# Kernel optimization log

Hardware: AMD Instinct MI355X
Metric: run time of the kernel (lower is better)

Reference implementation:

```python
import jax, jax.numpy as jnp
import numpy as np

THRESHOLD_FACTOR = 1.25
HIDDEN = 128
B, N = 4, 2048

def setup_inputs() -> dict:
    key = jax.random.key(0)
    ks = jax.random.split(key, 11)
    def lin(k, fin, fout):
        bound = 1.0 / np.sqrt(fin)
        kw, kb = jax.random.split(k)
        W = jax.random.uniform(kw, (fin, fout), jnp.float32, -bound, bound)
        b = jax.random.uniform(kb, (fout,), jnp.float32, -bound, bound)
        return W, b
    W1, b1 = lin(ks[0], 2, HIDDEN)
    W2, b2 = lin(ks[1], HIDDEN, HIDDEN)
    Wd, bd = lin(ks[2], HIDDEN, 1)
    Wr, br = lin(ks[3], HIDDEN, 1)
    Wm, bm = lin(ks[4], HIDDEN, 1)
    phase_coords = jax.random.normal(ks[5], (B, N, 2), jnp.float32)
    return dict(phase_coords=phase_coords, W1=W1, b1=b1, W2=W2, b2=b2,
                Wd=Wd, bd=bd, Wr=Wr, br=br, Wm=Wm, bm=bm)

def _attention(r):
    # diff[b,s,t,i] = r[b,s,i]*(-r[b,t,i]) + r[b,s,i] = r_s * (1 - r_t)
    diff = r[:, :, None, :] * (1.0 - r[:, None, :, :])        # [B,N,N,2]
    dist_sq = jnp.sum(diff * diff, axis=-1)                    # [B,N,N]
    phase_diff = jnp.arctan2(diff[..., 1], diff[..., 0])
    forward_bias = 0.5 * (1.0 + jnp.cos(phase_diff)) * jnp.exp(-dist_sq)
    mean_dist = jnp.mean(dist_sq, axis=(-1, -2), keepdims=True)
    std_dist = jnp.clip(jnp.std(dist_sq, axis=(-1, -2), keepdims=True, ddof=1), 1e-6, None)
    threshold = mean_dist + THRESHOLD_FACTOR * std_dist
    attn = jnp.where(dist_sq <= threshold, forward_bias, 0.0)
    row_sums = jnp.sum(attn, axis=-1, keepdims=True)
    return attn / (row_sums + 1e-8)

def reference(phase_coords, W1, b1, W2, b2, Wd, bd, Wr, br, Wm, bm):
    h = jax.nn.silu(phase_coords @ W1 + b1) @ W2 + b2           # [B,N,H]
    diffusion = h @ Wd + bd                                     # [B,N,1]
    reaction = h @ Wr + br
    migration = h @ Wm + bm
    attn = _attention(phase_coords)                             # [B,N,N]
    diffusion_field = jnp.einsum('bst,btk->bsk', attn, diffusion)
    return diffusion, reaction, migration, attn, diffusion_field
```

## Files before the change

kernel.cpp:

```cpp
#include <hip/hip_runtime.h>
#include <math.h>

#define NTOK 2048
#define HID  128
#define BB   4

typedef float f32x4 __attribute__((ext_vector_type(4)));

__device__ __forceinline__ float wave_red_f(float v) {
  #pragma unroll
  for (int o = 32; o; o >>= 1) v += __shfl_down(v, o, 64);
  return v;
}
__device__ __forceinline__ double wave_red_d(double v) {
  #pragma unroll
  for (int o = 32; o; o >>= 1) v += __shfl_down(v, o, 64);
  return v;
}

__global__ __launch_bounds__(256) void mlp_thr_kernel(
    const float* __restrict__ pc,
    const float* __restrict__ W1, const float* __restrict__ b1,
    const float* __restrict__ W2, const float* __restrict__ b2,
    const float* __restrict__ Wd, const float* __restrict__ bd,
    const float* __restrict__ Wr, const float* __restrict__ br,
    const float* __restrict__ Wm, const float* __restrict__ bm,
    float* __restrict__ outd, float* __restrict__ outr, float* __restrict__ outm,
    float* __restrict__ thr)
{
  const int tid = threadIdx.x;

  if (blockIdx.x >= 32) {
    const int wave = tid >> 6, lane = tid & 63;
    const int b = blockIdx.x - 32;
    const float2* r = (const float2*)(pc + (size_t)b * NTOK * 2);
    double m[10];
    #pragma unroll
    for (int j = 0; j < 10; ++j) m[j] = 0.0;
    for (int i = tid; i < NTOK; i += 256) {
      const float2 c = r[i];
      const double a = c.x, bq = c.y, u = 1.0 - (double)c.x, v = 1.0 - (double)c.y;
      const double a2 = a * a, b2v = bq * bq, u2 = u * u, v2 = v * v;
      m[0] += a2;       m[1] += b2v;
      m[2] += a2 * a2;  m[3] += b2v * b2v;  m[4] += a2 * b2v;
      m[5] += u2;       m[6] += v2;
      m[7] += u2 * u2;  m[8] += v2 * v2;    m[9] += u2 * v2;
    }
    #pragma unroll
    for (int j = 0; j < 10; ++j) m[j] = wave_red_d(m[j]);
    __shared__ double sm[4][10];
    if (lane == 0) {
      #pragma unroll
      for (int j = 0; j < 10; ++j) sm[wave][j] = m[j];
    }
    __syncthreads();
    if (tid == 0) {
      double t[10];
      #pragma unroll
      for (int j = 0; j < 10; ++j)
        t[j] = sm[0][j] + sm[1][j] + sm[2][j] + sm[3][j];
      const double Sq  = t[0] * t[5] + t[1] * t[6];
      const double Sqq = t[2] * t[7] + 2.0 * t[4] * t[9] + t[3] * t[8];
      const double M = (double)NTOK * (double)NTOK;
      const double mean = Sq / M;
      double var = (Sqq - Sq * Sq / M) / (M - 1.0);
      if (var < 0.0) var = 0.0;
      double sd = sqrt(var);
      if (sd < 1e-6) sd = 1e-6;
      thr[b] = (float)(mean + 1.25 * sd);
    }
    return;
  }

  __shared__ float fw[3][HID];
  __shared__ float fc[3];

  for (int idx = tid; idx < 3 * HID; idx += 256) {
    const int head = idx >> 7, k = idx & (HID - 1);
    const float* wh = (head == 0) ? Wd : (head == 1) ? Wr : Wm;
    const float4* w2row = (const float4*)(W2 + k * HID);
    const float4* wh4   = (const float4*)wh;
    float s = 0.f;
    #pragma unroll 4
    for (int j = 0; j < HID / 4; ++j) {
      const float4 a = w2row[j], w = wh4[j];
      s = fmaf(a.x, w.x, fmaf(a.y, w.y, fmaf(a.z, w.z, fmaf(a.w, w.w, s))));
    }
    fw[head][k] = s;
  }
  if (tid < 3) {
    const float* wh = (tid == 0) ? Wd : (tid == 1) ? Wr : Wm;
    const float bh  = (tid == 0) ? bd[0] : (tid == 1) ? br[0] : bm[0];
    const float4* b24 = (const float4*)b2;
    const float4* wh4 = (const float4*)wh;
    float s = 0.f;
    for (int j = 0; j < HID / 4; ++j) {
      const float4 a = b24[j], w = wh4[j];
      s = fmaf(a.x, w.x, fmaf(a.y, w.y, fmaf(a.z, w.z, fmaf(a.w, w.w, s))));
    }
    fc[tid] = s + bh;
  }
  __syncthreads();

  const int row = blockIdx.x * 256 + tid;
  const float2 c = ((const float2*)pc)[row];
  const float x0 = c.x, x1 = c.y;

  float dd = 0.f, rv = 0.f, mv = 0.f;
  #pragma unroll 4
  for (int k = 0; k < HID; ++k) {
    const float z = fmaf(x0, W1[k], fmaf(x1, W1[HID + k], b1[k]));
    const float h = z * __builtin_amdgcn_rcpf(1.f + __builtin_amdgcn_exp2f(-1.442695041f * z));
    dd = fmaf(h, fw[0][k], dd);
    rv = fmaf(h, fw[1][k], rv);
    mv = fmaf(h, fw[2][k], mv);
  }
  outd[row] = dd + fc[0];
  outr[row] = rv + fc[1];
  outm[row] = mv + fc[2];
}

__global__ __launch_bounds__(256) void attn_kernel(
    const float* __restrict__ pc, const float* __restrict__ diffu,
    const float* __restrict__ thr,
    float* __restrict__ attn, float* __restrict__ dfield)
{
  const int b = blockIdx.y;
  const int wave = threadIdx.x >> 6, lane = threadIdx.x & 63;
  const int s = blockIdx.x * 4 + wave;

  const float2* __restrict__ rr  = (const float2*)(pc + (size_t)b * NTOK * 2);
  const float4* __restrict__ rr4 = (const float4*)rr;
  const float4* __restrict__ sd4 = (const float4*)(diffu + b * NTOK);

  const float C = 1.2011224f;
  float2 u[32];
  float  sdr[32];
  #pragma unroll
  for (int j = 0; j < 8; ++j) {
    const float4 c0 = rr4[lane * 2 + j * 128];
    const float4 c1 = rr4[lane * 2 + 1 + j * 128];
    u[j * 4 + 0] = make_float2(C * (1.f - c0.x), C * (1.f - c0.y));
    u[j * 4 + 1] = make_float2(C * (1.f - c0.z), C * (1.f - c0.w));
    u[j * 4 + 2] = make_float2(C * (1.f - c1.x), C * (1.f - c1.y));
    u[j * 4 + 3] = make_float2(C * (1.f - c1.z), C * (1.f - c1.w));
    const float4 dv = sd4[lane + j * 64];
    sdr[j * 4 + 0] = dv.x; sdr[j * 4 + 1] = dv.y;
    sdr[j * 4 + 2] = dv.z; sdr[j * 4 + 3] = dv.w;
  }

  const float Ts = thr[b] * 1.442695041f;
  const float2 rc = rr[s];

  float v[32];
  float rsum = 0.f, dot = 0.f;
  #pragma unroll
  for (int k = 0; k < 32; ++k) {
    const float d0 = rc.x * u[k].x;
    const float d1 = rc.y * u[k].y;
    const float q = fmaf(d0, d0, d1 * d1);
    float val = 0.f;
    if (q <= Ts)
      val = (q > 0.f)
          ? fmaf(d0 * rsqrtf(q), 0.5f, 0.5f) * __builtin_amdgcn_exp2f(-q)
          : 1.f;
    v[k] = val;
    rsum += val;
    dot = fmaf(val, sdr[k], dot);
  }

  #pragma unroll
  for (int o = 1; o < 64; o <<= 1) {
    rsum += __shfl_xor(rsum, o, 64);
    dot  += __shfl_xor(dot, o, 64);
  }
  const float sc = 1.f / (rsum + 1e-8f);

  f32x4* arow4 = (f32x4*)(attn + ((size_t)b * NTOK + s) * NTOK);
  #pragma unroll
  for (int j = 0; j < 8; ++j) {
    f32x4 o;
    o.x = v[j * 4 + 0] * sc; o.y = v[j * 4 + 1] * sc;
    o.z = v[j * 4 + 2] * sc; o.w = v[j * 4 + 3] * sc;
    __builtin_nontemporal_store(o, arow4 + lane + j * 64);
  }
  if (lane == 0) dfield[b * NTOK + s] = dot * sc;
}

extern "C" void kernel_launch(void* const* d_in, const int* in_sizes, int n_in,
                              void* d_out, int out_size, void* d_ws, size_t ws_size,
                              hipStream_t stream) {
  const float* pc = (const float*)d_in[0];
  const float* W1 = (const float*)d_in[1];
  const float* b1 = (const float*)d_in[2];
  const float* W2 = (const float*)d_in[3];
  const float* b2 = (const float*)d_in[4];
  const float* Wd = (const float*)d_in[5];
  const float* bd = (const float*)d_in[6];
  const float* Wr = (const float*)d_in[7];
  const float* br = (const float*)d_in[8];
  const float* Wm = (const float*)d_in[9];
  const float* bm = (const float*)d_in[10];

  float* out    = (float*)d_out;
  float* outd   = out;
  float* outr   = out + BB * NTOK;
  float* outm   = out + 2 * BB * NTOK;
  float* attn   = out + 3 * BB * NTOK;
  float* dfield = attn + (size_t)BB * NTOK * NTOK;

  float* thr = (float*)d_ws;

  hipLaunchKernelGGL(mlp_thr_kernel, dim3(32 + BB), dim3(256), 0, stream,
                     pc, W1, b1, W2, b2, Wd, bd, Wr, br, Wm, bm,
                     outd, outr, outm, thr);
  hipLaunchKernelGGL(attn_kernel, dim3(NTOK / 4, BB), dim3(256), 0, stream,
                     pc, outd, thr, attn, dfield);
}
```

Measured before the change: 35.90 us.

## Split attention into row-stats pass and separate recompute-and-store pass

The fused attention kernel is split in two. A row-stats kernel computes the row sums and diffusion field and writes the per-row scale to a workspace buffer. A separate store kernel, with a flat grid-stride layout, recomputes every attention value and writes the normalized rows with plain stores instead of nontemporal ones. The aim is a cleaner, fully coalesced write stream for the 64 MB output, at the cost of computing each attention value twice and adding one kernel launch.

```diff
diff --git a/kernel.cpp b/kernel.cpp
--- a/kernel.cpp
+++ b/kernel.cpp
@@ -7,11 +7,6 @@
 
 typedef float f32x4 __attribute__((ext_vector_type(4)));
 
-__device__ __forceinline__ float wave_red_f(float v) {
-  #pragma unroll
-  for (int o = 32; o; o >>= 1) v += __shfl_down(v, o, 64);
-  return v;
-}
 __device__ __forceinline__ double wave_red_d(double v) {
   #pragma unroll
   for (int o = 32; o; o >>= 1) v += __shfl_down(v, o, 64);
@@ -120,10 +115,10 @@
   outm[row] = mv + fc[2];
 }
 
-__global__ __launch_bounds__(256) void attn_kernel(
+__global__ __launch_bounds__(256) void rowstats_kernel(
     const float* __restrict__ pc, const float* __restrict__ diffu,
     const float* __restrict__ thr,
-    float* __restrict__ attn, float* __restrict__ dfield)
+    float* __restrict__ scbuf, float* __restrict__ dfield)
 {
   const int b = blockIdx.y;
   const int wave = threadIdx.x >> 6, lane = threadIdx.x & 63;
@@ -152,7 +147,6 @@
   const float Ts = thr[b] * 1.442695041f;
   const float2 rc = rr[s];
 
-  float v[32];
   float rsum = 0.f, dot = 0.f;
   #pragma unroll
   for (int k = 0; k < 32; ++k) {
@@ -164,7 +158,6 @@
       val = (q > 0.f)
           ? fmaf(d0 * rsqrtf(q), 0.5f, 0.5f) * __builtin_amdgcn_exp2f(-q)
           : 1.f;
-    v[k] = val;
     rsum += val;
     dot = fmaf(val, sdr[k], dot);
   }
@@ -174,17 +167,54 @@
     rsum += __shfl_xor(rsum, o, 64);
     dot  += __shfl_xor(dot, o, 64);
   }
-  const float sc = 1.f / (rsum + 1e-8f);
-
-  f32x4* arow4 = (f32x4*)(attn + ((size_t)b * NTOK + s) * NTOK);
-  #pragma unroll
-  for (int j = 0; j < 8; ++j) {
+  if (lane == 0) {
+    const float sc = 1.f / (rsum + 1e-8f);
+    scbuf[b * NTOK + s]  = sc;
+    dfield[b * NTOK + s] = dot * sc;
+  }
+}
+
+#define C_TOTAL (BB * NTOK * (NTOK / 4))
+#define C_STRIDE (2048 * 256)
+__global__ __launch_bounds__(256) void store_kernel(
+    const float* __restrict__ pc, const float* __restrict__ thr,
+    const float* __restrict__ scbuf, float* __restrict__ attn)
+{
+  const float C = 1.2011224f;
+  const int tid0 = blockIdx.x * 256 + threadIdx.x;
+  f32x4* __restrict__ out4 = (f32x4*)attn;
+
+  #pragma unroll
+  for (int it = 0; it < C_TOTAL / C_STRIDE; ++it) {
+    const int idx = tid0 + it * C_STRIDE;
+    const int b   = idx >> 20;
+    const int r   = idx & 1048575;
+    const int s   = r >> 9;
+    const int t4  = r & 511;
+
+    const float2 rc = ((const float2*)pc)[(b << 11) + s];
+    const float4 c0 = ((const float4*)pc)[(b << 10) + t4 * 2];
+    const float4 c1 = ((const float4*)pc)[(b << 10) + t4 * 2 + 1];
+    const float Ts  = thr[b] * 1.442695041f;
+    const float scv = scbuf[(b << 11) + s];
+
     f32x4 o;
-    o.x = v[j * 4 + 0] * sc; o.y = v[j * 4 + 1] * sc;
-    o.z = v[j * 4 + 2] * sc; o.w = v[j * 4 + 3] * sc;
-    __builtin_nontemporal_store(o, arow4 + lane + j * 64);
-  }
-  if (lane == 0) dfield[b * NTOK + s] = dot * sc;
+    #pragma unroll
+    for (int j = 0; j < 4; ++j) {
+      const float cx = (j == 0) ? c0.x : (j == 1) ? c0.z : (j == 2) ? c1.x : c1.z;
+      const float cy = (j == 0) ? c0.y : (j == 1) ? c0.w : (j == 2) ? c1.y : c1.w;
+      const float d0 = rc.x * fmaf(-C, cx, C);
+      const float d1 = rc.y * fmaf(-C, cy, C);
+      const float q  = fmaf(d0, d0, d1 * d1);
+      float val = 0.f;
+      if (q <= Ts)
+        val = (q > 0.f)
+            ? fmaf(d0 * rsqrtf(q), 0.5f, 0.5f) * __builtin_amdgcn_exp2f(-q)
+            : 1.f;
+      o[j] = val * scv;
+    }
+    out4[idx] = o;
+  }
 }
 
 extern "C" void kernel_launch(void* const* d_in, const int* in_sizes, int n_in,
@@ -209,11 +239,14 @@
   float* attn   = out + 3 * BB * NTOK;
   float* dfield = attn + (size_t)BB * NTOK * NTOK;
 
-  float* thr = (float*)d_ws;
+  float* thr   = (float*)d_ws;
+  float* scbuf = thr + BB;
 
   hipLaunchKernelGGL(mlp_thr_kernel, dim3(32 + BB), dim3(256), 0, stream,
                      pc, W1, b1, W2, b2, Wd, bd, Wr, br, Wm, bm,
                      outd, outr, outm, thr);
-  hipLaunchKernelGGL(attn_kernel, dim3(NTOK / 4, BB), dim3(256), 0, stream,
-                     pc, outd, thr, attn, dfield);
-}
+  hipLaunchKernelGGL(rowstats_kernel, dim3(NTOK / 4, BB), dim3(256), 0, stream,
+                     pc, outd, thr, scbuf, dfield);
+  hipLaunchKernelGGL(store_kernel, dim3(2048), dim3(256), 0, stream,
+                     pc, thr, scbuf, attn);
+}
```

Measured after the change: 50.92 us. +41.8%, slower.
